# Kernel tuning notes

Measured on AMD Instinct MI355X. Metric: run time of the kernel, lower is better.

Reference implementation:

```python
import jax, jax.numpy as jnp
import numpy as np

P, N, D, H, AN, F = 20000, 16, 128, 8, 5, 512
DH = D // H  # 16


def layer_norm(x, g, b, eps=1e-5):
    m = jnp.mean(x, axis=-1, keepdims=True)
    v = jnp.var(x, axis=-1, keepdims=True)
    return (x - m) / jnp.sqrt(v + eps) * g + b


def setup_inputs() -> dict:
    key = jax.random.key(0)
    ks = jax.random.split(key, 12)
    s = 0.02
    return {
        "tgt": jax.random.normal(ks[0], (P, D * AN), jnp.float32),
        "index_pair": jax.random.randint(ks[1], (P, N), 0, P, jnp.int64),
        "cnt": P,
        "dist_atten": jax.random.normal(ks[2], (P, N, H), jnp.float32),
        "Wq": jax.random.normal(ks[3], (D, D), jnp.float32) * s,
        "Wk": jax.random.normal(ks[4], (D, D), jnp.float32) * s,
        "Wo": jax.random.normal(ks[5], (D, D), jnp.float32) * s,
        "W1": jax.random.normal(ks[6], (F, D), jnp.float32) * s,
        "b1f": jnp.zeros((F,), jnp.float32),
        "W2": jax.random.normal(ks[7], (D, F), jnp.float32) * s,
        "b2f": jnp.zeros((D,), jnp.float32),
        "g1": jnp.ones((D,), jnp.float32),
        "be1": jnp.zeros((D,), jnp.float32),
        "g2": jnp.ones((D,), jnp.float32),
        "be2": jnp.zeros((D,), jnp.float32),
    }


def reference(tgt, index_pair, cnt, dist_atten, Wq, Wk, Wo, W1, b1f, W2, b2f, g1, be1, g2, be2):
    x = tgt.reshape(P, D, AN)                       # [P, D, an]
    # Linear applied along D (torch Linear: y = x W^T), acting per equivariant channel an
    q = jnp.einsum('pea,de->pda', x, Wq)
    k = jnp.einsum('pea,de->pda', x, Wk)
    v = jnp.einsum('pea,de->pda', x, Wq)            # source uses to_q for value (faithful)
    # irregular neighbor gather (sa_attention_mapper_v3)
    kg = k.reshape(P, D * AN)[index_pair].reshape(P, N, H, DH, AN)
    vg = v.reshape(P, D * AN)[index_pair].reshape(P, N, H, DH, AN)
    qh = q.reshape(P, H, DH, AN)
    dot = jnp.einsum('phdi,pnhdi->pnh', qh, kg)     # [P, N, H]
    att = jax.nn.softmax((dot + dist_atten) / np.sqrt(DH).astype(np.float32), axis=1)
    t2 = jnp.einsum('pnh,pnhci->phci', att, vg).reshape(P, D, AN)
    t2 = jnp.einsum('pea,de->pda', t2, Wo)
    y = (x + t2).transpose(0, 2, 1)                 # [P, an, D]
    y = layer_norm(y, g1, be1)
    ff = jnp.maximum(y @ W1.T + b1f, 0.0) @ W2.T + b2f
    y = layer_norm(y + ff, g2, be2)
    return y.transpose(0, 2, 1).reshape(P, D * AN)
```

## Files before the change

### kernel.cpp

```cpp
#include <hip/hip_runtime.h>

#define PP   20000
#define NN   16
#define DD   128
#define HH   8
#define ANC  5
#define FF   512
#define PD   640
#define ROWS (PP * ANC)
#define KSTRIDE 648
#define SEG  20480


typedef __attribute__((ext_vector_type(8))) short  bf8;
typedef __attribute__((ext_vector_type(8))) unsigned short ushort8;
typedef __attribute__((ext_vector_type(4))) unsigned short us4;
typedef __attribute__((ext_vector_type(4))) float  f32x4;

__device__ inline float bf2f(unsigned short u) {
  union { unsigned int i; float f; } v; v.i = ((unsigned int)u) << 16; return v.f;
}
__device__ inline unsigned short f2bf(float f) {
  union { float f; unsigned int i; } v; v.f = f;
  unsigned int r = v.i + 0x7FFFu + ((v.i >> 16) & 1u);
  return (unsigned short)(r >> 16);
}

__global__ void k_wconv(const float* __restrict__ Wo, const float* __restrict__ W1,
                        const float* __restrict__ W2, const float* __restrict__ Wq,
                        const float* __restrict__ Wk,
                        unsigned short* __restrict__ Wob, unsigned short* __restrict__ W1b,
                        unsigned short* __restrict__ W2b, unsigned short* __restrict__ Wqb,
                        unsigned short* __restrict__ Wkb)
{
  int i = blockIdx.x * 256 + threadIdx.x;
  if (i < 16384) { Wob[i] = f2bf(Wo[i]); Wqb[i] = f2bf(Wq[i]); Wkb[i] = f2bf(Wk[i]); }
  if (i < 65536) { W1b[i] = f2bf(W1[i]); W2b[i] = f2bf(W2[i]); }
}

__global__ __launch_bounds__(320) void k_xpose(
    const float* __restrict__ tgt, unsigned short* __restrict__ xb)
{
  __shared__ float xs[5 * 1032];
  const int t = threadIdx.x;
  const int p0 = blockIdx.x * 8;
  const float* src = tgt + (size_t)p0 * PD;
#pragma unroll
  for (int i = 0; i < 16; ++i) {
    int lin = t + i * 320;
    float v = src[lin];
    int pt = lin / PD;
    int rem = lin - pt * PD;
    int e = rem / 5;
    int a = rem - e * 5;
    xs[a * 1032 + e * 8 + pt] = v;
  }
  __syncthreads();
  const size_t base = (size_t)(blockIdx.x >> 1) * SEG + (size_t)(blockIdx.x & 1) * 5120;
  for (int i = t; i < 5120; i += 320) {
    int row_l = i >> 7, col = i & 127;
    int pt = row_l / 5, a = row_l - pt * 5;
    xb[base + i] = f2bf(xs[a * 1032 + col * 8 + pt]);
  }
}

__global__ __launch_bounds__(256) void k_qk_gemm(
    const unsigned short* __restrict__ xb, const unsigned short* __restrict__ Wqb,
    const unsigned short* __restrict__ Wkb, unsigned short* __restrict__ kqb)
{
  __shared__ unsigned short Sb[80 * 136];
  const int t = threadIdx.x;
  const int w = t >> 6, l = t & 63;
  const int lc = l & 15, kg = l >> 4;
  const int p0 = blockIdx.x * 16;
  const unsigned short* xseg = xb + (size_t)blockIdx.x * SEG;

  f32x4 zq[5][2], zk[5][2];
#pragma unroll
  for (int m = 0; m < 5; ++m)
#pragma unroll
    for (int n = 0; n < 2; ++n) {
      zq[m][n] = (f32x4){0.f, 0.f, 0.f, 0.f};
      zk[m][n] = (f32x4){0.f, 0.f, 0.f, 0.f};
    }
  bf8 wq[2][4], wk[2][4];
#pragma unroll
  for (int nt = 0; nt < 2; ++nt)
#pragma unroll
    for (int kf = 0; kf < 4; ++kf) {
      size_t wo = (size_t)((2 * w + nt) * 16 + lc) * DD + kf * 32 + kg * 8;
      wq[nt][kf] = *reinterpret_cast<const bf8*>(&Wqb[wo]);
      wk[nt][kf] = *reinterpret_cast<const bf8*>(&Wkb[wo]);
    }
#pragma unroll
  for (int mt = 0; mt < 5; ++mt) {
    const unsigned short* ap = xseg + (mt * 16 + lc) * DD + kg * 8;
    bf8 a0 = *reinterpret_cast<const bf8*>(ap);
    bf8 a1 = *reinterpret_cast<const bf8*>(ap + 32);
    bf8 a2 = *reinterpret_cast<const bf8*>(ap + 64);
    bf8 a3 = *reinterpret_cast<const bf8*>(ap + 96);
#pragma unroll
    for (int nt = 0; nt < 2; ++nt) {
      zq[mt][nt] = __builtin_amdgcn_mfma_f32_16x16x32_bf16(a0, wq[nt][0], zq[mt][nt], 0, 0, 0);
      zq[mt][nt] = __builtin_amdgcn_mfma_f32_16x16x32_bf16(a1, wq[nt][1], zq[mt][nt], 0, 0, 0);
      zq[mt][nt] = __builtin_amdgcn_mfma_f32_16x16x32_bf16(a2, wq[nt][2], zq[mt][nt], 0, 0, 0);
      zq[mt][nt] = __builtin_amdgcn_mfma_f32_16x16x32_bf16(a3, wq[nt][3], zq[mt][nt], 0, 0, 0);
      zk[mt][nt] = __builtin_amdgcn_mfma_f32_16x16x32_bf16(a0, wk[nt][0], zk[mt][nt], 0, 0, 0);
      zk[mt][nt] = __builtin_amdgcn_mfma_f32_16x16x32_bf16(a1, wk[nt][1], zk[mt][nt], 0, 0, 0);
      zk[mt][nt] = __builtin_amdgcn_mfma_f32_16x16x32_bf16(a2, wk[nt][2], zk[mt][nt], 0, 0, 0);
      zk[mt][nt] = __builtin_amdgcn_mfma_f32_16x16x32_bf16(a3, wk[nt][3], zk[mt][nt], 0, 0, 0);
    }
  }
#pragma unroll
  for (int mt = 0; mt < 5; ++mt)
#pragma unroll
    for (int j = 0; j < 4; ++j)
#pragma unroll
      for (int nt = 0; nt < 2; ++nt)
        Sb[(mt * 16 + kg * 4 + j) * 136 + (2 * w + nt) * 16 + lc] = f2bf(zq[mt][nt][j]);
  __syncthreads();
  for (int i = t; i < 10240; i += 256) {
    int pl = i / 640, rem = i - pl * 640;
    int d = rem / 5, a = rem - d * 5;
    kqb[(size_t)(p0 + pl) * 1280 + 640 + rem] = Sb[(pl * 5 + a) * 136 + d];
  }
  __syncthreads();
#pragma unroll
  for (int mt = 0; mt < 5; ++mt)
#pragma unroll
    for (int j = 0; j < 4; ++j)
#pragma unroll
      for (int nt = 0; nt < 2; ++nt)
        Sb[(mt * 16 + kg * 4 + j) * 136 + (2 * w + nt) * 16 + lc] = f2bf(zk[mt][nt][j]);
  __syncthreads();
  for (int i = t; i < 10240; i += 256) {
    int pl = i / 640, rem = i - pl * 640;
    int d = rem / 5, a = rem - d * 5;
    kqb[(size_t)(p0 + pl) * 1280 + rem] = Sb[(pl * 5 + a) * 136 + d];
  }
}

__global__ __launch_bounds__(256, 4) void k_attn(
    const unsigned short* __restrict__ kqb, const int* __restrict__ idx,
    const float* __restrict__ dist, unsigned short* __restrict__ t2b)
{
  __shared__ unsigned short ksh[NN * KSTRIDE];
  __shared__ unsigned short qsh[648];
  __shared__ float sc[128];
  __shared__ float att[128];
  __shared__ int sidx[NN];
  const int t = threadIdx.x;
  const int p = blockIdx.x;
  if (t < NN) sidx[t] = idx[p * NN + t];
  if (t < 80)
    *reinterpret_cast<ushort8*>(&qsh[t * 8]) =
        *reinterpret_cast<const ushort8*>(&kqb[(size_t)p * 1280 + 640 + t * 8]);
  float dv = 0.f;
  if (t < 128) dv = dist[(size_t)p * 128 + (t & 15) * 8 + (t >> 4)];
  __syncthreads();
  us4 vreg[16];
  const int o0 = (t < 160) ? t * 4 : 0;
  if (t < 160) {
#pragma unroll
    for (int n = 0; n < 16; ++n)
      vreg[n] = *reinterpret_cast<const us4*>(&kqb[(size_t)sidx[n] * 1280 + 640 + o0]);
  }
#pragma unroll
  for (int it = 0; it < 5; ++it) {
    int u = t + it * 256;
    int n = u / 80, c = u - n * 80;
    *reinterpret_cast<ushort8*>(&ksh[n * KSTRIDE + c * 8]) =
        *reinterpret_cast<const ushort8*>(&kqb[(size_t)sidx[n] * 1280 + c * 8]);
  }
  __syncthreads();
  if (t < 128) {
    int n = t & 15, h = t >> 4;
    const unsigned short* kp = &ksh[n * KSTRIDE + h * 80];
    const unsigned short* qp = &qsh[h * 80];
    float acc = 0.f;
#pragma unroll
    for (int j = 0; j < 10; ++j) {
      ushort8 kv8 = *reinterpret_cast<const ushort8*>(&kp[j * 8]);
      ushort8 qv8 = *reinterpret_cast<const ushort8*>(&qp[j * 8]);
#pragma unroll
      for (int jj = 0; jj < 8; ++jj) acc += bf2f(kv8[jj]) * bf2f(qv8[jj]);
    }
    sc[h * 16 + n] = (acc + dv) * 0.25f;
  }
  __syncthreads();
  if (t < 8) {
    float m = -1e30f;
#pragma unroll
    for (int n = 0; n < 16; ++n) m = fmaxf(m, sc[t * 16 + n]);
    float s = 0.f;
    float ev[16];
#pragma unroll
    for (int n = 0; n < 16; ++n) { ev[n] = __expf(sc[t * 16 + n] - m); s += ev[n]; }
    float inv = 1.f / s;
#pragma unroll
    for (int n = 0; n < 16; ++n) att[t * 16 + n] = ev[n] * inv;
  }
  __syncthreads();
  if (t < 160) {
    const int h = o0 / 80;
    float facc[4] = {0.f, 0.f, 0.f, 0.f};
#pragma unroll
    for (int n = 0; n < 16; ++n) {
      float aw = att[h * 16 + n];
#pragma unroll
      for (int j = 0; j < 4; ++j) facc[j] += aw * bf2f(vreg[n][j]);
    }
    unsigned short* t2p = t2b + (size_t)(p >> 4) * SEG + 10240 + ((p & 15) * 5) * 128;
#pragma unroll
    for (int j = 0; j < 4; ++j) {
      int o = o0 + j;
      int e = o / 5, a = o - e * 5;
      t2p[a * 128 + e] = f2bf(facc[j]);
    }
  }
}

__global__ __launch_bounds__(256, 2) void k_ffn_mfma(
    float* out, const unsigned short* __restrict__ Wob,
    const unsigned short* __restrict__ W1b, const float* __restrict__ b1,
    const unsigned short* __restrict__ W2b, const float* __restrict__ b2,
    const float* __restrict__ g1, const float* __restrict__ be1,
    const float* __restrict__ g2, const float* __restrict__ be2)
{
  __shared__ unsigned short SH[2 * 80 * 136];
  __shared__ float mrow[80], rrow[80];
  unsigned short* Yb = SH;
  unsigned short* Hb = SH + 80 * 136;
  const int t = threadIdx.x;
  const int w = t >> 6, l = t & 63;
  const int lc = l & 15;
  const int kg = l >> 4;
  const int c0 = (2 * w) * 16 + lc;
  const int c1 = c0 + 16;
  const unsigned short* xseg = (const unsigned short*)out + (size_t)blockIdx.x * SEG;
  const unsigned short* t2seg = xseg + 10240;

  f32x4 zac[5][2];
#pragma unroll
  for (int m = 0; m < 5; ++m)
#pragma unroll
    for (int n = 0; n < 2; ++n) zac[m][n] = (f32x4){0.f, 0.f, 0.f, 0.f};

  {
    bf8 wb[2][4];
#pragma unroll
    for (int nt = 0; nt < 2; ++nt)
#pragma unroll
      for (int kf = 0; kf < 4; ++kf)
        wb[nt][kf] = *reinterpret_cast<const bf8*>(
            &Wob[(size_t)((2 * w + nt) * 16 + lc) * DD + kf * 32 + kg * 8]);
#pragma unroll
    for (int mt = 0; mt < 5; ++mt) {
      const unsigned short* ap = t2seg + (mt * 16 + lc) * DD + kg * 8;
      bf8 a0 = *reinterpret_cast<const bf8*>(ap);
      bf8 a1 = *reinterpret_cast<const bf8*>(ap + 32);
      bf8 a2 = *reinterpret_cast<const bf8*>(ap + 64);
      bf8 a3 = *reinterpret_cast<const bf8*>(ap + 96);
#pragma unroll
      for (int nt = 0; nt < 2; ++nt) {
        zac[mt][nt] = __builtin_amdgcn_mfma_f32_16x16x32_bf16(a0, wb[nt][0], zac[mt][nt], 0, 0, 0);
        zac[mt][nt] = __builtin_amdgcn_mfma_f32_16x16x32_bf16(a1, wb[nt][1], zac[mt][nt], 0, 0, 0);
        zac[mt][nt] = __builtin_amdgcn_mfma_f32_16x16x32_bf16(a2, wb[nt][2], zac[mt][nt], 0, 0, 0);
        zac[mt][nt] = __builtin_amdgcn_mfma_f32_16x16x32_bf16(a3, wb[nt][3], zac[mt][nt], 0, 0, 0);
      }
    }
  }
#pragma unroll
  for (int mt = 0; mt < 5; ++mt) {
    int rb = mt * 16 + kg * 4;
#pragma unroll
    for (int j = 0; j < 4; ++j) {
      int row = rb + j;
      zac[mt][0][j] += bf2f(xseg[row * DD + c0]);
      zac[mt][1][j] += bf2f(xseg[row * DD + c1]);
      Yb[row * 136 + c0] = f2bf(zac[mt][0][j]);
      Yb[row * 136 + c1] = f2bf(zac[mt][1][j]);
    }
  }
  __syncthreads();
  if (t < 160) {
    int row = t >> 1, hf = t & 1;
    const unsigned short* rp = Yb + row * 136 + hf * 64;
    float s = 0.f, s2 = 0.f;
#pragma unroll
    for (int c8 = 0; c8 < 8; ++c8) {
      bf8 v8 = *reinterpret_cast<const bf8*>(rp + c8 * 8);
#pragma unroll
      for (int j = 0; j < 8; ++j) {
        float f = bf2f((unsigned short)v8[j]);
        s += f; s2 += f * f;
      }
    }
    s += __shfl_xor(s, 1); s2 += __shfl_xor(s2, 1);
    if (!hf) {
      float mm = s * (1.f / 128.f);
      float vv = s2 * (1.f / 128.f) - mm * mm;
      mrow[row] = mm;
      rrow[row] = rsqrtf(vv + 1e-5f);
    }
  }
  __syncthreads();
  {
    float g1a = g1[c0], g1b = g1[c1], e1a = be1[c0], e1b = be1[c1];
#pragma unroll
    for (int mt = 0; mt < 5; ++mt) {
      int rb = mt * 16 + kg * 4;
#pragma unroll
      for (int j = 0; j < 4; ++j) {
        int row = rb + j;
        float mm = mrow[row], rr = rrow[row];
        float y0 = (zac[mt][0][j] - mm) * rr * g1a + e1a;
        float y1 = (zac[mt][1][j] - mm) * rr * g1b + e1b;
        zac[mt][0][j] = y0; zac[mt][1][j] = y1;
        Yb[row * 136 + c0] = f2bf(y0);
        Yb[row * 136 + c1] = f2bf(y1);
      }
    }
  }
  __syncthreads();
  f32x4 oac[5][2];
#pragma unroll
  for (int m = 0; m < 5; ++m)
#pragma unroll
    for (int n = 0; n < 2; ++n) oac[m][n] = (f32x4){0.f, 0.f, 0.f, 0.f};

  for (int c = 0; c < 4; ++c) {
    bf8 w1f[2][4];
#pragma unroll
    for (int nt = 0; nt < 2; ++nt)
#pragma unroll
      for (int kf = 0; kf < 4; ++kf)
        w1f[nt][kf] = *reinterpret_cast<const bf8*>(
            &W1b[(size_t)(c * 128 + (2 * w + nt) * 16 + lc) * DD + kf * 32 + kg * 8]);
    f32x4 hac[5][2];
#pragma unroll
    for (int m = 0; m < 5; ++m)
#pragma unroll
      for (int n = 0; n < 2; ++n) hac[m][n] = (f32x4){0.f, 0.f, 0.f, 0.f};
#pragma unroll
    for (int mt = 0; mt < 5; ++mt) {
      const unsigned short* yp = Yb + (mt * 16 + lc) * 136 + kg * 8;
      bf8 a0 = *reinterpret_cast<const bf8*>(yp);
      bf8 a1 = *reinterpret_cast<const bf8*>(yp + 32);
      bf8 a2 = *reinterpret_cast<const bf8*>(yp + 64);
      bf8 a3 = *reinterpret_cast<const bf8*>(yp + 96);
#pragma unroll
      for (int nt = 0; nt < 2; ++nt) {
        hac[mt][nt] = __builtin_amdgcn_mfma_f32_16x16x32_bf16(a0, w1f[nt][0], hac[mt][nt], 0, 0, 0);
        hac[mt][nt] = __builtin_amdgcn_mfma_f32_16x16x32_bf16(a1, w1f[nt][1], hac[mt][nt], 0, 0, 0);
        hac[mt][nt] = __builtin_amdgcn_mfma_f32_16x16x32_bf16(a2, w1f[nt][2], hac[mt][nt], 0, 0, 0);
        hac[mt][nt] = __builtin_amdgcn_mfma_f32_16x16x32_bf16(a3, w1f[nt][3], hac[mt][nt], 0, 0, 0);
      }
    }
    float b1a = b1[c * 128 + c0], b1b = b1[c * 128 + c1];
    __syncthreads();
#pragma unroll
    for (int mt = 0; mt < 5; ++mt) {
      int rb = mt * 16 + kg * 4;
#pragma unroll
      for (int j = 0; j < 4; ++j) {
        int row = rb + j;
        Hb[row * 136 + c0] = f2bf(fmaxf(hac[mt][0][j] + b1a, 0.f));
        Hb[row * 136 + c1] = f2bf(fmaxf(hac[mt][1][j] + b1b, 0.f));
      }
    }
    __syncthreads();
    bf8 w2f[2][4];
#pragma unroll
    for (int nt = 0; nt < 2; ++nt)
#pragma unroll
      for (int kf = 0; kf < 4; ++kf)
        w2f[nt][kf] = *reinterpret_cast<const bf8*>(
            &W2b[(size_t)((2 * w + nt) * 16 + lc) * FF + c * 128 + kf * 32 + kg * 8]);
#pragma unroll
    for (int mt = 0; mt < 5; ++mt) {
      const unsigned short* hp = Hb + (mt * 16 + lc) * 136 + kg * 8;
      bf8 a0 = *reinterpret_cast<const bf8*>(hp);
      bf8 a1 = *reinterpret_cast<const bf8*>(hp + 32);
      bf8 a2 = *reinterpret_cast<const bf8*>(hp + 64);
      bf8 a3 = *reinterpret_cast<const bf8*>(hp + 96);
#pragma unroll
      for (int nt = 0; nt < 2; ++nt) {
        oac[mt][nt] = __builtin_amdgcn_mfma_f32_16x16x32_bf16(a0, w2f[nt][0], oac[mt][nt], 0, 0, 0);
        oac[mt][nt] = __builtin_amdgcn_mfma_f32_16x16x32_bf16(a1, w2f[nt][1], oac[mt][nt], 0, 0, 0);
        oac[mt][nt] = __builtin_amdgcn_mfma_f32_16x16x32_bf16(a2, w2f[nt][2], oac[mt][nt], 0, 0, 0);
        oac[mt][nt] = __builtin_amdgcn_mfma_f32_16x16x32_bf16(a3, w2f[nt][3], oac[mt][nt], 0, 0, 0);
      }
    }
  }
  __syncthreads();
  {
    float b2a = b2[c0], b2b = b2[c1];
#pragma unroll
    for (int mt = 0; mt < 5; ++mt) {
      int rb = mt * 16 + kg * 4;
#pragma unroll
      for (int j = 0; j < 4; ++j) {
        int row = rb + j;
        float v0 = zac[mt][0][j] + oac[mt][0][j] + b2a;
        float v1 = zac[mt][1][j] + oac[mt][1][j] + b2b;
        oac[mt][0][j] = v0; oac[mt][1][j] = v1;
        Yb[row * 136 + c0] = f2bf(v0);
        Yb[row * 136 + c1] = f2bf(v1);
      }
    }
  }
  __syncthreads();
  if (t < 160) {
    int row = t >> 1, hf = t & 1;
    const unsigned short* rp = Yb + row * 136 + hf * 64;
    float s = 0.f, s2 = 0.f;
#pragma unroll
    for (int c8 = 0; c8 < 8; ++c8) {
      bf8 v8 = *reinterpret_cast<const bf8*>(rp + c8 * 8);
#pragma unroll
      for (int j = 0; j < 8; ++j) {
        float f = bf2f((unsigned short)v8[j]);
        s += f; s2 += f * f;
      }
    }
    s += __shfl_xor(s, 1); s2 += __shfl_xor(s2, 1);
    if (!hf) {
      float mm = s * (1.f / 128.f);
      float vv = s2 * (1.f / 128.f) - mm * mm;
      mrow[row] = mm;
      rrow[row] = rsqrtf(vv + 1e-5f);
    }
  }
  __syncthreads();
  {
    float* fb = (float*)SH;
    float g2a = g2[c0], g2b = g2[c1], e2a = be2[c0], e2b = be2[c1];
#pragma unroll
    for (int mt = 0; mt < 5; ++mt) {
      int rb = mt * 16 + kg * 4;
#pragma unroll
      for (int j = 0; j < 4; ++j) {
        int row = rb + j;
        float mm = mrow[row], rr = rrow[row];
        fb[row * 132 + c0] = (oac[mt][0][j] - mm) * rr * g2a + e2a;
        fb[row * 132 + c1] = (oac[mt][1][j] - mm) * rr * g2b + e2b;
      }
    }
    __syncthreads();
    const size_t ob = (size_t)blockIdx.x * 16 * PD;
    for (int i = t; i < 10240; i += 256) {
      int pl = i / PD, rem = i - pl * PD;
      int d = rem / 5, a = rem - d * 5;
      out[ob + i] = fb[(pl * 5 + a) * 132 + d];
    }
  }
}

extern "C" void kernel_launch(void* const* d_in, const int* in_sizes, int n_in,
                              void* d_out, int out_size, void* d_ws, size_t ws_size,
                              hipStream_t stream) {
  (void)in_sizes; (void)n_in; (void)out_size; (void)ws_size;
  const float* tgt  = (const float*)d_in[0];
  const int*   idx  = (const int*)d_in[1];
  const float* dist = (const float*)d_in[3];
  const float* Wq   = (const float*)d_in[4];
  const float* Wk   = (const float*)d_in[5];
  const float* Wo   = (const float*)d_in[6];
  const float* W1   = (const float*)d_in[7];
  const float* b1f  = (const float*)d_in[8];
  const float* W2   = (const float*)d_in[9];
  const float* b2f  = (const float*)d_in[10];
  const float* g1   = (const float*)d_in[11];
  const float* be1  = (const float*)d_in[12];
  const float* g2   = (const float*)d_in[13];
  const float* be2  = (const float*)d_in[14];
  float* out = (float*)d_out;

  unsigned short* kqb = (unsigned short*)d_ws;
  unsigned short* Wob = kqb + (size_t)PP * 1280;
  unsigned short* W1b = Wob + DD * DD;
  unsigned short* W2b = W1b + FF * DD;
  unsigned short* Wqb = W2b + FF * DD;
  unsigned short* Wkb = Wqb + DD * DD;
  unsigned short* ovl = (unsigned short*)d_out;

  k_wconv  <<<256, 256, 0, stream>>>(Wo, W1, W2, Wq, Wk, Wob, W1b, W2b, Wqb, Wkb);
  k_xpose  <<<PP / 8, 320, 0, stream>>>(tgt, ovl);
  k_qk_gemm<<<ROWS / 80, 256, 0, stream>>>(ovl, Wqb, Wkb, kqb);
  k_attn   <<<PP, 256, 0, stream>>>(kqb, idx, dist, ovl);
  k_ffn_mfma<<<ROWS / 80, 256, 0, stream>>>(out, Wob, W1b, b1f, W2b, b2f,
                                            g1, be1, g2, be2);
}
```

Before: 356.9 us.

## Store gathered K and V in fp8 and read K directly from global in attention

```diff
diff --git a/kernel.cpp b/kernel.cpp
--- a/kernel.cpp
+++ b/kernel.cpp
@@ -8,7 +8,6 @@
 #define FF   512
 #define PD   640
 #define ROWS (PP * ANC)
-#define KSTRIDE 648
 #define SEG  20480
 
 
@@ -66,7 +65,8 @@
 
 __global__ __launch_bounds__(256) void k_qk_gemm(
     const unsigned short* __restrict__ xb, const unsigned short* __restrict__ Wqb,
-    const unsigned short* __restrict__ Wkb, unsigned short* __restrict__ kqb)
+    const unsigned short* __restrict__ Wkb, unsigned char* __restrict__ kq8,
+    unsigned short* __restrict__ qb16)
 {
   __shared__ unsigned short Sb[80 * 136];
   const int t = threadIdx.x;
@@ -119,10 +119,21 @@
       for (int nt = 0; nt < 2; ++nt)
         Sb[(mt * 16 + kg * 4 + j) * 136 + (2 * w + nt) * 16 + lc] = f2bf(zq[mt][nt][j]);
   __syncthreads();
-  for (int i = t; i < 10240; i += 256) {
+  for (int i = t * 4; i < 10240; i += 1024) {
     int pl = i / 640, rem = i - pl * 640;
-    int d = rem / 5, a = rem - d * 5;
-    kqb[(size_t)(p0 + pl) * 1280 + 640 + rem] = Sb[(pl * 5 + a) * 136 + d];
+    unsigned short u[4]; float f[4];
+#pragma unroll
+    for (int j = 0; j < 4; ++j) {
+      int o = rem + j; int d = o / 5, a = o - d * 5;
+      u[j] = Sb[(pl * 5 + a) * 136 + d];
+      f[j] = bf2f(u[j]);
+    }
+    us4 uv = {u[0], u[1], u[2], u[3]};
+    *reinterpret_cast<us4*>(&qb16[(size_t)(p0 + pl) * 640 + rem]) = uv;
+    int wd = 0;
+    wd = __builtin_amdgcn_cvt_pk_fp8_f32(f[0], f[1], wd, false);
+    wd = __builtin_amdgcn_cvt_pk_fp8_f32(f[2], f[3], wd, true);
+    *reinterpret_cast<int*>(&kq8[(size_t)(p0 + pl) * 1280 + 640 + rem]) = wd;
   }
   __syncthreads();
 #pragma unroll
@@ -133,19 +144,27 @@
       for (int nt = 0; nt < 2; ++nt)
         Sb[(mt * 16 + kg * 4 + j) * 136 + (2 * w + nt) * 16 + lc] = f2bf(zk[mt][nt][j]);
   __syncthreads();
-  for (int i = t; i < 10240; i += 256) {
+  for (int i = t * 4; i < 10240; i += 1024) {
     int pl = i / 640, rem = i - pl * 640;
-    int d = rem / 5, a = rem - d * 5;
-    kqb[(size_t)(p0 + pl) * 1280 + rem] = Sb[(pl * 5 + a) * 136 + d];
-  }
-}
-
-__global__ __launch_bounds__(256, 4) void k_attn(
-    const unsigned short* __restrict__ kqb, const int* __restrict__ idx,
-    const float* __restrict__ dist, unsigned short* __restrict__ t2b)
+    float f[4];
+#pragma unroll
+    for (int j = 0; j < 4; ++j) {
+      int o = rem + j; int d = o / 5, a = o - d * 5;
+      f[j] = bf2f(Sb[(pl * 5 + a) * 136 + d]);
+    }
+    int wd = 0;
+    wd = __builtin_amdgcn_cvt_pk_fp8_f32(f[0], f[1], wd, false);
+    wd = __builtin_amdgcn_cvt_pk_fp8_f32(f[2], f[3], wd, true);
+    *reinterpret_cast<int*>(&kq8[(size_t)(p0 + pl) * 1280 + rem]) = wd;
+  }
+}
+
+__global__ __launch_bounds__(256, 6) void k_attn(
+    const unsigned char* __restrict__ kq8, const unsigned short* __restrict__ qb16,
+    const int* __restrict__ idx, const float* __restrict__ dist,
+    unsigned short* __restrict__ t2b)
 {
-  __shared__ unsigned short ksh[NN * KSTRIDE];
-  __shared__ unsigned short qsh[648];
+  __shared__ unsigned short qsh[640];
   __shared__ float sc[128];
   __shared__ float att[128];
   __shared__ int sidx[NN];
@@ -154,36 +173,44 @@
   if (t < NN) sidx[t] = idx[p * NN + t];
   if (t < 80)
     *reinterpret_cast<ushort8*>(&qsh[t * 8]) =
-        *reinterpret_cast<const ushort8*>(&kqb[(size_t)p * 1280 + 640 + t * 8]);
+        *reinterpret_cast<const ushort8*>(&qb16[(size_t)p * 640 + t * 8]);
   float dv = 0.f;
   if (t < 128) dv = dist[(size_t)p * 128 + (t & 15) * 8 + (t >> 4)];
   __syncthreads();
-  us4 vreg[16];
+  unsigned vbits[16];
   const int o0 = (t < 160) ? t * 4 : 0;
   if (t < 160) {
 #pragma unroll
     for (int n = 0; n < 16; ++n)
-      vreg[n] = *reinterpret_cast<const us4*>(&kqb[(size_t)sidx[n] * 1280 + 640 + o0]);
-  }
-#pragma unroll
-  for (int it = 0; it < 5; ++it) {
-    int u = t + it * 256;
-    int n = u / 80, c = u - n * 80;
-    *reinterpret_cast<ushort8*>(&ksh[n * KSTRIDE + c * 8]) =
-        *reinterpret_cast<const ushort8*>(&kqb[(size_t)sidx[n] * 1280 + c * 8]);
-  }
-  __syncthreads();
+      vbits[n] = *reinterpret_cast<const unsigned*>(
+          &kq8[(size_t)sidx[n] * 1280 + 640 + o0]);
+  }
   if (t < 128) {
     int n = t & 15, h = t >> 4;
-    const unsigned short* kp = &ksh[n * KSTRIDE + h * 80];
+    const unsigned char* kp = &kq8[(size_t)sidx[n] * 1280 + h * 80];
     const unsigned short* qp = &qsh[h * 80];
     float acc = 0.f;
 #pragma unroll
-    for (int j = 0; j < 10; ++j) {
-      ushort8 kv8 = *reinterpret_cast<const ushort8*>(&kp[j * 8]);
-      ushort8 qv8 = *reinterpret_cast<const ushort8*>(&qp[j * 8]);
-#pragma unroll
-      for (int jj = 0; jj < 8; ++jj) acc += bf2f(kv8[jj]) * bf2f(qv8[jj]);
+    for (int j4 = 0; j4 < 5; ++j4) {
+      uint4 kw = *reinterpret_cast<const uint4*>(kp + j4 * 16);
+      ushort8 qa = *reinterpret_cast<const ushort8*>(qp + j4 * 16);
+      ushort8 qb = *reinterpret_cast<const ushort8*>(qp + j4 * 16 + 8);
+      acc += __builtin_amdgcn_cvt_f32_fp8(kw.x, 0) * bf2f(qa[0]);
+      acc += __builtin_amdgcn_cvt_f32_fp8(kw.x, 1) * bf2f(qa[1]);
+      acc += __builtin_amdgcn_cvt_f32_fp8(kw.x, 2) * bf2f(qa[2]);
+      acc += __builtin_amdgcn_cvt_f32_fp8(kw.x, 3) * bf2f(qa[3]);
+      acc += __builtin_amdgcn_cvt_f32_fp8(kw.y, 0) * bf2f(qa[4]);
+      acc += __builtin_amdgcn_cvt_f32_fp8(kw.y, 1) * bf2f(qa[5]);
+      acc += __builtin_amdgcn_cvt_f32_fp8(kw.y, 2) * bf2f(qa[6]);
+      acc += __builtin_amdgcn_cvt_f32_fp8(kw.y, 3) * bf2f(qa[7]);
+      acc += __builtin_amdgcn_cvt_f32_fp8(kw.z, 0) * bf2f(qb[0]);
+      acc += __builtin_amdgcn_cvt_f32_fp8(kw.z, 1) * bf2f(qb[1]);
+      acc += __builtin_amdgcn_cvt_f32_fp8(kw.z, 2) * bf2f(qb[2]);
+      acc += __builtin_amdgcn_cvt_f32_fp8(kw.z, 3) * bf2f(qb[3]);
+      acc += __builtin_amdgcn_cvt_f32_fp8(kw.w, 0) * bf2f(qb[4]);
+      acc += __builtin_amdgcn_cvt_f32_fp8(kw.w, 1) * bf2f(qb[5]);
+      acc += __builtin_amdgcn_cvt_f32_fp8(kw.w, 2) * bf2f(qb[6]);
+      acc += __builtin_amdgcn_cvt_f32_fp8(kw.w, 3) * bf2f(qb[7]);
     }
     sc[h * 16 + n] = (acc + dv) * 0.25f;
   }
@@ -207,8 +234,10 @@
 #pragma unroll
     for (int n = 0; n < 16; ++n) {
       float aw = att[h * 16 + n];
-#pragma unroll
-      for (int j = 0; j < 4; ++j) facc[j] += aw * bf2f(vreg[n][j]);
+      facc[0] += aw * __builtin_amdgcn_cvt_f32_fp8(vbits[n], 0);
+      facc[1] += aw * __builtin_amdgcn_cvt_f32_fp8(vbits[n], 1);
+      facc[2] += aw * __builtin_amdgcn_cvt_f32_fp8(vbits[n], 2);
+      facc[3] += aw * __builtin_amdgcn_cvt_f32_fp8(vbits[n], 3);
     }
     unsigned short* t2p = t2b + (size_t)(p >> 4) * SEG + 10240 + ((p & 15) * 5) * 128;
 #pragma unroll
@@ -477,18 +506,19 @@
   const float* be2  = (const float*)d_in[14];
   float* out = (float*)d_out;
 
-  unsigned short* kqb = (unsigned short*)d_ws;
-  unsigned short* Wob = kqb + (size_t)PP * 1280;
-  unsigned short* W1b = Wob + DD * DD;
-  unsigned short* W2b = W1b + FF * DD;
-  unsigned short* Wqb = W2b + FF * DD;
-  unsigned short* Wkb = Wqb + DD * DD;
-  unsigned short* ovl = (unsigned short*)d_out;
+  unsigned char*  kq8  = (unsigned char*)d_ws;
+  unsigned short* qb16 = (unsigned short*)(kq8 + (size_t)PP * 1280);
+  unsigned short* Wob  = qb16 + (size_t)PP * 640;
+  unsigned short* W1b  = Wob + DD * DD;
+  unsigned short* W2b  = W1b + FF * DD;
+  unsigned short* Wqb  = W2b + FF * DD;
+  unsigned short* Wkb  = Wqb + DD * DD;
+  unsigned short* ovl  = (unsigned short*)d_out;
 
   k_wconv  <<<256, 256, 0, stream>>>(Wo, W1, W2, Wq, Wk, Wob, W1b, W2b, Wqb, Wkb);
   k_xpose  <<<PP / 8, 320, 0, stream>>>(tgt, ovl);
-  k_qk_gemm<<<ROWS / 80, 256, 0, stream>>>(ovl, Wqb, Wkb, kqb);
-  k_attn   <<<PP, 256, 0, stream>>>(kqb, idx, dist, ovl);
+  k_qk_gemm<<<ROWS / 80, 256, 0, stream>>>(ovl, Wqb, Wkb, kq8, qb16);
+  k_attn   <<<PP, 256, 0, stream>>>(kq8, qb16, idx, dist, ovl);
   k_ffn_mfma<<<ROWS / 80, 256, 0, stream>>>(out, Wob, W1b, b1f, W2b, b2f,
                                             g1, be1, g2, be2);
 }
```

Result: faster. 316.6 us (-11.3%).
